# Kernel tuning notes

Hardware: AMD Instinct MI355X
Metric: run time of the kernel (lower is better)

## Reference

```python
import jax, jax.numpy as jnp
import numpy as np

N, F, HID, OUT, H = 4096, 128, 64, 16, 4
ALPHA = 0.2          # leaky relu slope
NEG = -9e15          # mask fill value (pyGAT convention)


def setup_inputs() -> dict:
    key = jax.random.key(0)
    ks = jax.random.split(key, 8)
    x = jax.random.normal(ks[0], (N, F), dtype=jnp.float32)
    adj = jax.random.randint(ks[1], (N, N), 0, 2, dtype=jnp.int32)
    s = lambda *sh: 0.1
    W_in = jax.random.normal(ks[2], (H, F, F), dtype=jnp.float32) * 0.1
    a_in = jax.random.normal(ks[3], (H, 2 * F), dtype=jnp.float32) * 0.1
    W_hid = jax.random.normal(ks[4], (H, F * H, HID), dtype=jnp.float32) * 0.1
    a_hid = jax.random.normal(ks[5], (H, 2 * HID), dtype=jnp.float32) * 0.1
    W_out = jax.random.normal(ks[6], (HID * H, OUT), dtype=jnp.float32) * 0.1
    a_out = jax.random.normal(ks[7], (2 * OUT,), dtype=jnp.float32) * 0.1
    return {"x": x, "adj": adj, "W_in": W_in, "a_in": a_in,
            "W_hid": W_hid, "a_hid": a_hid, "W_out": W_out, "a_out": a_out}


def _multi_head_att(x, W, a, mask):
    """Dense multi-head GAT aggregation. x:[N,Fin], W:[H,Fin,D], a:[H,2D] -> [H,N,D]."""
    D = W.shape[-1]
    h = jnp.einsum('nf,hfd->hnd', x, W)                      # [H,N,D]
    f1 = jnp.einsum('hnd,hd->hn', h, a[:, :D])               # source scores
    f2 = jnp.einsum('hnd,hd->hn', h, a[:, D:])               # target scores
    e = jax.nn.leaky_relu(f1[:, :, None] + f2[:, None, :], ALPHA)  # [H,N,N]
    e = jnp.where(mask[None, :, :], e, NEG)
    att = jax.nn.softmax(e, axis=-1)
    return jnp.einsum('hnm,hmd->hnd', att, h)                # [H,N,D]


def _concat_heads(h):
    # [H,N,D] -> [N,H*D]
    Hh, n, d = h.shape
    return jnp.transpose(h, (1, 0, 2)).reshape(n, Hh * d)


def reference(x, adj, W_in, a_in, W_hid, a_hid, W_out, a_out):
    mask = adj > 0
    # input attention block: concat=True (ELU per head), identity skip (in==out dim)
    h1 = _multi_head_att(x, W_in, a_in, mask)                # [H,N,F]
    h1 = jax.nn.elu(h1 + x[None, :, :])                      # identity residual
    h1 = _concat_heads(h1)                                   # [N,H*F]
    # hidden attention block: concat=True
    h2 = _multi_head_att(h1, W_hid, a_hid, mask)             # [H,N,HID]
    h2 = _concat_heads(jax.nn.elu(h2))                       # [N,H*HID]
    # output attention layer: single head, concat=False (no ELU inside)
    h3 = _multi_head_att(h2, W_out[None], a_out[None], mask)[0]  # [N,OUT]
    return jax.nn.log_softmax(jax.nn.elu(h3), axis=1)
```

## Files before the change

kernel.cpp:

```cpp
#include <hip/hip_runtime.h>
#include <math.h>

#define NN 4096
#define FF 128
#define HH 4
#define HIDD 64
#define OUTD 16
#define MASKW (NN / 32)
#define ALPHA 0.2f

typedef __attribute__((ext_vector_type(8))) short short8;
typedef __attribute__((ext_vector_type(4))) float f32x4;

__device__ __forceinline__ ushort f2bf(float f) {
    unsigned u = __float_as_uint(f);
    return (ushort)((u + 0x7fffu + ((u >> 16) & 1u)) >> 16);
}
__device__ __forceinline__ float bf2f(ushort u) {
    return __uint_as_float((unsigned)u << 16);
}

__global__ void pack_mask_kernel(const int* __restrict__ adj, unsigned int* __restrict__ mb) {
    int t = blockIdx.x * 256 + threadIdx.x;
    int v = adj[t] > 0;
    unsigned long long bal = __ballot(v);
    if ((threadIdx.x & 63) == 0) {
        int w = t >> 5;
        mb[w] = (unsigned int)(bal & 0xffffffffULL);
        mb[w + 1] = (unsigned int)(bal >> 32);
    }
}

__global__ void cvt_kernel(const float* __restrict__ x, ushort* __restrict__ xb) {
    int e = (blockIdx.x * 256 + threadIdx.x) * 4;
    f32x4 v = *(const f32x4*)&x[e];
    unsigned lo = (unsigned)f2bf(v[0]) | ((unsigned)f2bf(v[1]) << 16);
    unsigned hi = (unsigned)f2bf(v[2]) | ((unsigned)f2bf(v[3]) << 16);
    uint2 p; p.x = lo; p.y = hi;
    *(uint2*)&xb[e] = p;
}

__global__ void wtprep_kernel(const float* __restrict__ W_in, const float* __restrict__ W_hid,
                              const float* __restrict__ W_out,
                              ushort* __restrict__ wt1, ushort* __restrict__ wt2,
                              ushort* __restrict__ wt3) {
    int idx = blockIdx.x * 256 + threadIdx.x;
    if (idx < 65536) {
        int k = idx & 127, n = (idx >> 7) & 127, hd = idx >> 14;
        wt1[idx] = f2bf(W_in[((size_t)hd * 128 + k) * 128 + n]);
    } else if (idx < 65536 + 131072) {
        int j = idx - 65536;
        int k = j & 511, n = (j >> 9) & 63, hd = j >> 15;
        wt2[j] = f2bf(W_hid[((size_t)hd * 512 + k) * 64 + n]);
    } else if (idx < 65536 + 131072 + 4096) {
        int j = idx - 196608;
        int k = j & 255, n = j >> 8;
        wt3[j] = f2bf(W_out[(size_t)k * 16 + n]);
    }
}

__global__ void vprep_kernel(const float* __restrict__ W_in, const float* __restrict__ a_in,
                             const float* __restrict__ W_hid, const float* __restrict__ a_hid,
                             const float* __restrict__ W_out, const float* __restrict__ a_out,
                             float* __restrict__ vbuf) {
    int idx = blockIdx.x * 256 + threadIdx.x;
    const float* Wr; const float* ar; int D; float* dst;
    if (idx < 1024) {
        int f = idx & 127, hd = (idx >> 7) & 3, s = idx >> 9;
        Wr = W_in + ((size_t)hd * 128 + f) * 128;
        ar = a_in + hd * 256 + s * 128;
        D = 128; dst = &vbuf[idx];
    } else if (idx < 1024 + 4096) {
        int j = idx - 1024;
        int f = j & 511, hd = (j >> 9) & 3, s = j >> 11;
        Wr = W_hid + ((size_t)hd * 512 + f) * 64;
        ar = a_hid + hd * 128 + s * 64;
        D = 64; dst = &vbuf[1024 + j];
    } else if (idx < 1024 + 4096 + 512) {
        int j = idx - 5120;
        int f = j & 255, s = j >> 8;
        Wr = W_out + (size_t)f * 16;
        ar = a_out + s * 16;
        D = 16; dst = &vbuf[5120 + j];
    } else return;
    float s = 0.f;
    for (int d = 0; d < D; d++) s += Wr[d] * ar[d];
    *dst = s;
}

template <typename T, int K, int H>
__global__ __launch_bounds__(256) void score_kernel(const T* __restrict__ A,
                                                    const float* __restrict__ v,
                                                    float* __restrict__ f1,
                                                    float* __restrict__ f2) {
    int wv = blockIdx.x * 4 + (threadIdx.x >> 6);
    int lane = threadIdx.x & 63;
    int hd = wv >> 12;
    int i = wv & (NN - 1);
    const T* ar = A + (size_t)i * K;
    const float* v1r = v + (size_t)hd * K;
    const float* v2r = v + (size_t)(H + hd) * K;
    float s1 = 0.f, s2 = 0.f;
    for (int f = lane; f < K; f += 64) {
        float av;
        if constexpr (sizeof(T) == 2) av = bf2f(((const ushort*)ar)[f]);
        else av = ((const float*)ar)[f];
        s1 += av * v1r[f];
        s2 += av * v2r[f];
    }
#pragma unroll
    for (int o = 32; o > 0; o >>= 1) {
        s1 += __shfl_down(s1, o);
        s2 += __shfl_down(s2, o);
    }
    if (lane == 0) { f1[wv] = s1; f2[wv] = s2; }
}

__global__ void gmax_kernel(const float* __restrict__ f2, float* __restrict__ gmax) {
    int hd = blockIdx.x;
    const float* p = f2 + (size_t)hd * NN;
    float m = -1e30f;
    for (int i = threadIdx.x; i < NN; i += 256) m = fmaxf(m, p[i]);
    __shared__ float sm[4];
#pragma unroll
    for (int off = 32; off > 0; off >>= 1) m = fmaxf(m, __shfl_down(m, off));
    if ((threadIdx.x & 63) == 0) sm[threadIdx.x >> 6] = m;
    __syncthreads();
    if (threadIdx.x == 0) gmax[hd] = fmaxf(fmaxf(sm[0], sm[1]), fmaxf(sm[2], sm[3]));
}

template <int K, int N, int CFG>
__global__ __launch_bounds__(256) void proj_mfma_kernel(const ushort* __restrict__ A,
                                                        const ushort* __restrict__ WT,
                                                        ushort* __restrict__ hT) {
    constexpr int NT = (CFG == 0) ? (N / 64) : (N / 16);
    __shared__ ushort ts[4][NT * 16][20];
    const int hd = blockIdx.y;
    const int t = threadIdx.x;
    const int w = t >> 6, lane = t & 63, ln = lane & 15, g = lane >> 4, g8 = g * 8;
    const int i0 = (CFG == 0) ? blockIdx.x * 16 : blockIdx.x * 64 + w * 16;
    const int n0 = (CFG == 0) ? w * (N / 4) : 0;
    const ushort* WTh = WT + (size_t)hd * N * K;
    ushort* hTh = hT + (size_t)hd * N * NN;
    f32x4 acc[NT];
#pragma unroll
    for (int n = 0; n < NT; n++) acc[n] = (f32x4)(0.f);
    const ushort* arow = A + (size_t)(i0 + ln) * K + g8;
#pragma unroll
    for (int k0 = 0; k0 < K; k0 += 32) {
        short8 aF = *(const short8*)&arow[k0];
#pragma unroll
        for (int n = 0; n < NT; n++) {
            short8 bF = *(const short8*)&WTh[(size_t)(n0 + n * 16 + ln) * K + k0 + g8];
            acc[n] = __builtin_amdgcn_mfma_f32_16x16x32_bf16(aF, bF, acc[n], 0, 0, 0);
        }
    }
#pragma unroll
    for (int n = 0; n < NT; n++) {
        unsigned lo = (unsigned)f2bf(acc[n][0]) | ((unsigned)f2bf(acc[n][1]) << 16);
        unsigned hi = (unsigned)f2bf(acc[n][2]) | ((unsigned)f2bf(acc[n][3]) << 16);
        uint2 p; p.x = lo; p.y = hi;
        *(uint2*)&ts[w][n * 16 + ln][g * 4] = p;
    }
#pragma unroll
    for (int n = 0; n < NT; n++) {
        int d = lane >> 2, ip = lane & 3;
        uint2 rv = *(uint2*)&ts[w][n * 16 + d][ip * 4];
        *(uint2*)&hTh[(size_t)(n0 + n * 16 + d) * NN + i0 + ip * 4] = rv;
    }
}

template <int D>
__global__ __launch_bounds__(256) void agg3_kernel(const ushort* __restrict__ hT,
                                                   const float* __restrict__ f1,
                                                   const float* __restrict__ f2,
                                                   const float* __restrict__ gmax,
                                                   const unsigned int* __restrict__ mb,
                                                   float* __restrict__ pacc,
                                                   float* __restrict__ plsum) {
    constexpr int NT = D / 16;
    constexpr int NC = D / 64;
    __shared__ ushort hs[D][40];
    const int hd = blockIdx.z;
    const int js = blockIdx.y;
    const int jlen = NN / gridDim.y;
    const int jb = js * jlen, je = jb + jlen;
    const int t = threadIdx.x;
    const int w = t >> 6;
    const int lane = t & 63;
    const int ln = lane & 15;
    const int g = lane >> 4;
    const int g8 = g * 8;
    const int i0 = blockIdx.x * 64 + w * 16;
    const ushort* hTh = hT + (size_t)hd * D * NN;

    const float f1v = f1[hd * NN + i0 + ln];
    const float gm = gmax[hd];
    float mi = f1v + gm;
    mi = fmaxf(mi, ALPHA * mi);
    const float L2E = 1.442695040888963f;
    const float cexp = -mi * L2E;

    f32x4 acc[NT];
#pragma unroll
    for (int n = 0; n < NT; n++) acc[n] = (f32x4)(0.f);
    float lsum = 0.f;
    const float* f2h = f2 + hd * NN;
    const unsigned* mrow = mb + (size_t)(i0 + ln) * MASKW;

    int srow[NC], scol[NC];
#pragma unroll
    for (int c = 0; c < NC; c++) {
        int ch = t + c * 256;
        srow[c] = ch >> 2;
        scol[c] = (ch & 3) * 8;
    }
    uint4 st[NC];
#pragma unroll
    for (int c = 0; c < NC; c++)
        st[c] = *(const uint4*)&hTh[(size_t)srow[c] * NN + jb + scol[c]];
    unsigned mw = mrow[jb >> 5];
    f32x4 fA = *(const f32x4*)&f2h[jb + g8];
    f32x4 fB = *(const f32x4*)&f2h[jb + g8 + 4];

    for (int j0 = jb; j0 < je; j0 += 32) {
        __syncthreads();
#pragma unroll
        for (int c = 0; c < NC; c++) *(uint4*)&hs[srow[c]][scol[c]] = st[c];
        __syncthreads();
        const bool more = (j0 + 32) < je;
        if (more) {
#pragma unroll
            for (int c = 0; c < NC; c++)
                st[c] = *(const uint4*)&hTh[(size_t)srow[c] * NN + j0 + 32 + scol[c]];
        }
        unsigned bits = (mw >> g8) & 0xffu;
        f32x4 cA = fA, cB = fB;
        if (more) {
            mw = mrow[(j0 + 32) >> 5];
            fA = *(const f32x4*)&f2h[j0 + 32 + g8];
            fB = *(const f32x4*)&f2h[j0 + 32 + g8 + 4];
        }
        unsigned au[4];
#pragma unroll
        for (int tp = 0; tp < 4; tp++) {
            unsigned pu[2];
#pragma unroll
            for (int q = 0; q < 2; q++) {
                int tt = tp * 2 + q;
                float f2t = (tt < 4) ? cA[tt] : cB[tt - 4];
                float e = f1v + f2t;
                e = fmaxf(e, ALPHA * e);
                float p = ((bits >> tt) & 1u) ? __builtin_amdgcn_exp2f(e * L2E + cexp) : 0.f;
                pu[q] = __float_as_uint(p) & 0xffff0000u;
                lsum += __uint_as_float(pu[q]);
            }
            au[tp] = (pu[0] >> 16) | pu[1];
        }
        union { unsigned u[4]; short8 s; } aF;
#pragma unroll
        for (int q = 0; q < 4; q++) aF.u[q] = au[q];
#pragma unroll
        for (int n = 0; n < NT; n++) {
            short8 bF = *(const short8*)&hs[n * 16 + ln][g8];
            acc[n] = __builtin_amdgcn_mfma_f32_16x16x32_bf16(aF.s, bF, acc[n], 0, 0, 0);
        }
    }
    lsum += __shfl_xor(lsum, 16);
    lsum += __shfl_xor(lsum, 32);
    const size_t pbase = ((size_t)js * HH + hd) * NN;
    if (g == 0) plsum[pbase + i0 + ln] = lsum;
    float* pb = pacc + pbase * D;
#pragma unroll
    for (int n = 0; n < NT; n++) {
#pragma unroll
        for (int r = 0; r < 4; r++) {
            pb[(size_t)(i0 + g * 4 + r) * D + n * 16 + ln] = acc[n][r];
        }
    }
}

template <int D, int EPI>
__global__ __launch_bounds__(256) void combine_kernel(const float* __restrict__ pacc,
                                                      const float* __restrict__ plsum,
                                                      const float* __restrict__ xres,
                                                      ushort* __restrict__ out,
                                                      int ncols, int JS) {
    const int hd = blockIdx.y;
    const int e = (blockIdx.x * 256 + threadIdx.x) * 4;
    const int row = e / D;
    const int col = e % D;
    f32x4 s = (f32x4)(0.f);
    float l = 0.f;
    for (int js = 0; js < JS; js++) {
        const size_t pbase = ((size_t)js * HH + hd) * NN;
        s += *(const f32x4*)&pacc[(pbase + row) * D + col];
        l += plsum[pbase + row];
    }
    const float inv = 1.f / l;
    f32x4 xv;
    if (EPI == 1) xv = *(const f32x4*)&xres[(size_t)row * D + col];
    float o[4];
#pragma unroll
    for (int k = 0; k < 4; k++) {
        float v = s[k] * inv;
        if (EPI == 1) v += xv[k];
        if (EPI >= 1) v = v > 0.f ? v : (__expf(v) - 1.f);
        o[k] = v;
    }
    unsigned lo = (unsigned)f2bf(o[0]) | ((unsigned)f2bf(o[1]) << 16);
    unsigned hi = (unsigned)f2bf(o[2]) | ((unsigned)f2bf(o[3]) << 16);
    uint2 p; p.x = lo; p.y = hi;
    *(uint2*)&out[(size_t)row * ncols + hd * D + col] = p;
}

template <int D, int EPI>
__global__ __launch_bounds__(256) void agg2_kernel(const ushort* __restrict__ hT,
                                                   const float* __restrict__ f1,
                                                   const float* __restrict__ f2,
                                                   const float* __restrict__ gmax,
                                                   const unsigned int* __restrict__ mb,
                                                   const float* __restrict__ xres,
                                                   ushort* __restrict__ out, int ncols) {
    constexpr int NT = D / 16;
    constexpr int NC = D / 64;
    __shared__ ushort hs[D][40];
    const int hd = blockIdx.z;
    const int t = threadIdx.x;
    const int w = t >> 6;
    const int lane = t & 63;
    const int ln = lane & 15;
    const int g = lane >> 4;
    const int g8 = g * 8;
    const int i0 = blockIdx.x * 64 + w * 16;
    const ushort* hTh = hT + (size_t)hd * D * NN;
    const float f1v = f1[hd * NN + i0 + ln];
    const float gm = gmax[hd];
    float mi = f1v + gm;
    mi = fmaxf(mi, ALPHA * mi);
    const float L2E = 1.442695040888963f;
    const float cexp = -mi * L2E;
    f32x4 acc[NT];
#pragma unroll
    for (int n = 0; n < NT; n++) acc[n] = (f32x4)(0.f);
    float lsum = 0.f;
    const float* f2h = f2 + hd * NN;
    const unsigned* mrow = mb + (size_t)(i0 + ln) * MASKW;
    int srow[NC], scol[NC];
#pragma unroll
    for (int c = 0; c < NC; c++) {
        int ch = t + c * 256;
        srow[c] = ch >> 2;
        scol[c] = (ch & 3) * 8;
    }
    uint4 st[NC];
#pragma unroll
    for (int c = 0; c < NC; c++)
        st[c] = *(const uint4*)&hTh[(size_t)srow[c] * NN + scol[c]];
    unsigned mw = mrow[0];
    f32x4 fA = *(const f32x4*)&f2h[g8];
    f32x4 fB = *(const f32x4*)&f2h[g8 + 4];
    for (int j0 = 0; j0 < NN; j0 += 32) {
        __syncthreads();
#pragma unroll
        for (int c = 0; c < NC; c++) *(uint4*)&hs[srow[c]][scol[c]] = st[c];
        __syncthreads();
        const bool more = (j0 + 32) < NN;
        if (more) {
#pragma unroll
            for (int c = 0; c < NC; c++)
                st[c] = *(const uint4*)&hTh[(size_t)srow[c] * NN + j0 + 32 + scol[c]];
        }
        unsigned bits = (mw >> g8) & 0xffu;
        f32x4 cA = fA, cB = fB;
        if (more) {
            mw = mrow[(j0 + 32) >> 5];
            fA = *(const f32x4*)&f2h[j0 + 32 + g8];
            fB = *(const f32x4*)&f2h[j0 + 32 + g8 + 4];
        }
        unsigned au[4];
#pragma unroll
        for (int tp = 0; tp < 4; tp++) {
            unsigned pu[2];
#pragma unroll
            for (int q = 0; q < 2; q++) {
                int tt = tp * 2 + q;
                float f2t = (tt < 4) ? cA[tt] : cB[tt - 4];
                float e = f1v + f2t;
                e = fmaxf(e, ALPHA * e);
                float p = ((bits >> tt) & 1u) ? __builtin_amdgcn_exp2f(e * L2E + cexp) : 0.f;
                pu[q] = __float_as_uint(p) & 0xffff0000u;
                lsum += __uint_as_float(pu[q]);
            }
            au[tp] = (pu[0] >> 16) | pu[1];
        }
        union { unsigned u[4]; short8 s; } aF;
#pragma unroll
        for (int q = 0; q < 4; q++) aF.u[q] = au[q];
#pragma unroll
        for (int n = 0; n < NT; n++) {
            short8 bF = *(const short8*)&hs[n * 16 + ln][g8];
            acc[n] = __builtin_amdgcn_mfma_f32_16x16x32_bf16(aF.s, bF, acc[n], 0, 0, 0);
        }
    }
    lsum += __shfl_xor(lsum, 16);
    lsum += __shfl_xor(lsum, 32);
    const float linv = 1.f / lsum;
#pragma unroll
    for (int n = 0; n < NT; n++) {
#pragma unroll
        for (int r = 0; r < 4; r++) {
            float invr = __shfl(linv, (g << 2) + r);
            float v = acc[n][r] * invr;
            int row = i0 + g * 4 + r;
            int col = n * 16 + ln;
            if (EPI == 1) v += xres[(size_t)row * D + col];
            if (EPI >= 1) v = v > 0.f ? v : (__expf(v) - 1.f);
            out[(size_t)row * ncols + hd * D + col] = f2bf(v);
        }
    }
}

template <int D, int EPI, int NW>
__global__ __launch_bounds__(NW * 64) void agg_mfma_kernel(const ushort* __restrict__ hT,
                                                           const float* __restrict__ f1,
                                                           const float* __restrict__ f2,
                                                           const float* __restrict__ gmax,
                                                           const unsigned int* __restrict__ mb,
                                                           const float* __restrict__ xres,
                                                           float* __restrict__ out, int ncols) {
    constexpr int NT = D / 16;
    static_assert(NW == 1 || NT == 1, "j-split only for single-tile D");
    const int hd = blockIdx.z;
    const int i0 = blockIdx.x * 16;
    const int w = threadIdx.x >> 6;
    const int lane = threadIdx.x & 63;
    const int ln = lane & 15;
    const int g = lane >> 4;
    const int g8 = g * 8;
    const ushort* hTh = hT + (size_t)hd * D * NN;
    const float f1v = f1[hd * NN + i0 + ln];
    const float gm = gmax[hd];
    float mi = f1v + gm;
    mi = fmaxf(mi, ALPHA * mi);
    f32x4 acc[NT];
#pragma unroll
    for (int n = 0; n < NT; n++) acc[n] = (f32x4)(0.f);
    float lsum = 0.f;
    const float* f2h = f2 + hd * NN;
    const unsigned* mrow = mb + (size_t)(i0 + ln) * MASKW;
    const int jbeg = w * (NN / NW), jend = jbeg + NN / NW;

    for (int j0 = jbeg; j0 < jend; j0 += 32) {
        unsigned bits = (mrow[j0 >> 5] >> g8) & 0xffu;
        f32x4 fA = *(const f32x4*)&f2h[j0 + g8];
        f32x4 fB = *(const f32x4*)&f2h[j0 + g8 + 4];
        short8 aF;
#pragma unroll
        for (int t = 0; t < 8; t++) {
            float f2t = (t < 4) ? fA[t] : fB[t - 4];
            float e = f1v + f2t;
            e = fmaxf(e, ALPHA * e);
            float p = ((bits >> t) & 1u) ? __expf(e - mi) : 0.f;
            ushort pb = f2bf(p);
            aF[t] = (short)pb;
            lsum += __uint_as_float((unsigned)pb << 16);
        }
#pragma unroll
        for (int n = 0; n < NT; n++) {
            short8 bF = *(const short8*)&hTh[(size_t)(n * 16 + ln) * NN + j0 + g8];
            acc[n] = __builtin_amdgcn_mfma_f32_16x16x32_bf16(aF, bF, acc[n], 0, 0, 0);
        }
    }
    lsum += __shfl_xor(lsum, 16);
    lsum += __shfl_xor(lsum, 32);

    float accF[NT][4];
    float ltot;
    __shared__ float accL[NW][16][17];
    __shared__ float lsL[NW][16];
    if constexpr (NW == 1) {
#pragma unroll
        for (int n = 0; n < NT; n++)
#pragma unroll
            for (int r = 0; r < 4; r++) accF[n][r] = acc[n][r];
        ltot = lsum;
    } else {
#pragma unroll
        for (int r = 0; r < 4; r++) accL[w][g * 4 + r][ln] = acc[0][r];
        if (lane < 16) lsL[w][lane] = lsum;
        __syncthreads();
        if (w != 0) return;
#pragma unroll
        for (int r = 0; r < 4; r++) {
            float s = 0.f;
            for (int ww = 0; ww < NW; ww++) s += accL[ww][g * 4 + r][ln];
            accF[0][r] = s;
        }
        float s = 0.f;
        for (int ww = 0; ww < NW; ww++) s += lsL[ww][ln];
        ltot = s;
    }
    const float linv = 1.f / ltot;
#pragma unroll
    for (int n = 0; n < NT; n++) {
#pragma unroll
        for (int r = 0; r < 4; r++) {
            float invr = __shfl(linv, (g << 2) + r);
            float v = accF[n][r] * invr;
            int row = i0 + g * 4 + r;
            int col = n * 16 + ln;
            if (EPI == 1) v += xres[(size_t)row * D + col];
            if (EPI >= 1) v = v > 0.f ? v : (__expf(v) - 1.f);
            out[(size_t)row * ncols + hd * D + col] = v;
        }
    }
}

__global__ void final_kernel(const float* __restrict__ h3, float* __restrict__ out) {
    int i = blockIdx.x * 256 + threadIdx.x;
    if (i >= NN) return;
    float v[OUTD];
    float mx = -1e30f;
#pragma unroll
    for (int k = 0; k < OUTD; k++) {
        float e = h3[(size_t)i * OUTD + k];
        e = e > 0.f ? e : (__expf(e) - 1.f);
        v[k] = e;
        mx = fmaxf(mx, e);
    }
    float s = 0.f;
#pragma unroll
    for (int k = 0; k < OUTD; k++) s += __expf(v[k] - mx);
    float ls = logf(s);
#pragma unroll
    for (int k = 0; k < OUTD; k++) out[(size_t)i * OUTD + k] = v[k] - mx - ls;
}

extern "C" void kernel_launch(void* const* d_in, const int* in_sizes, int n_in,
                              void* d_out, int out_size, void* d_ws, size_t ws_size,
                              hipStream_t stream) {
    const float* x = (const float*)d_in[0];
    const int* adj = (const int*)d_in[1];
    const float* W_in = (const float*)d_in[2];
    const float* a_in = (const float*)d_in[3];
    const float* W_hid = (const float*)d_in[4];
    const float* a_hid = (const float*)d_in[5];
    const float* W_out = (const float*)d_in[6];
    const float* a_out = (const float*)d_in[7];
    float* out = (float*)d_out;

    char* w = (char*)d_ws;
    unsigned int* mb = (unsigned int*)w;  w += (size_t)NN * MASKW * 4;
    ushort* hT = (ushort*)w;              w += (size_t)HH * NN * FF * 2;
    ushort* xb16 = (ushort*)w;            w += (size_t)NN * FF * 2;
    ushort* cat1b = (ushort*)w;           w += (size_t)NN * (HH * FF) * 2;
    ushort* cat2b = (ushort*)w;           w += (size_t)NN * (HH * HIDD) * 2;
    ushort* wt1 = (ushort*)w;             w += 65536 * 2;
    ushort* wt2 = (ushort*)w;             w += 131072 * 2;
    ushort* wt3 = (ushort*)w;             w += 4096 * 2;
    float* vbuf = (float*)w;              w += 5632 * 4;
    float* f1 = (float*)w;                w += (size_t)HH * NN * 4;
    float* f2 = (float*)w;                w += (size_t)HH * NN * 4;
    float* gm = (float*)w;                w += 256;
    float* h3 = (float*)w;                w += (size_t)NN * OUTD * 4;
    size_t base_used = (size_t)(w - (char*)d_ws);

    int JS = 0;
    float* pacc = (float*)w;
    float* plsum = nullptr;
    {
        size_t per_js = (size_t)HH * NN * FF * 4;
        size_t ls_per_js = (size_t)HH * NN * 4;
        for (int cand = 4; cand >= 1; cand >>= 1) {
            size_t need = base_used + (size_t)cand * per_js + (size_t)(2 * cand) * ls_per_js + 1024;
            if (ws_size >= need) { JS = cand; break; }
        }
        if (JS) plsum = (float*)((char*)pacc + (size_t)JS * per_js);
    }
    const int JS2 = 2 * JS;

    hipLaunchKernelGGL(pack_mask_kernel, dim3(NN * NN / 256), dim3(256), 0, stream, adj, mb);
    hipLaunchKernelGGL(cvt_kernel, dim3(NN * FF / 1024), dim3(256), 0, stream, x, xb16);
    hipLaunchKernelGGL(wtprep_kernel, dim3(784), dim3(256), 0, stream,
                       W_in, W_hid, W_out, wt1, wt2, wt3);
    hipLaunchKernelGGL(vprep_kernel, dim3(22), dim3(256), 0, stream,
                       W_in, a_in, W_hid, a_hid, W_out, a_out, vbuf);

    hipLaunchKernelGGL((proj_mfma_kernel<FF, FF, 0>), dim3(NN / 16, HH), dim3(256), 0, stream,
                       xb16, wt1, hT);
    hipLaunchKernelGGL((score_kernel<float, FF, HH>), dim3(HH * NN / 4), dim3(256), 0, stream,
                       x, vbuf, f1, f2);
    hipLaunchKernelGGL(gmax_kernel, dim3(HH), dim3(256), 0, stream, f2, gm);
    if (JS) {
        hipLaunchKernelGGL((agg3_kernel<FF>), dim3(NN / 64, JS, HH), dim3(256), 0, stream,
                           hT, f1, f2, gm, mb, pacc, plsum);
        hipLaunchKernelGGL((combine_kernel<FF, 1>), dim3(NN * FF / 1024, HH), dim3(256), 0, stream,
                           pacc, plsum, x, cat1b, HH * FF, JS);
    } else {
        hipLaunchKernelGGL((agg2_kernel<FF, 1>), dim3(NN / 64, 1, HH), dim3(256), 0, stream,
                           hT, f1, f2, gm, mb, x, cat1b, HH * FF);
    }

    hipLaunchKernelGGL((proj_mfma_kernel<HH * FF, HIDD, 0>), dim3(NN / 16, HH), dim3(256), 0, stream,
                       cat1b, wt2, hT);
    hipLaunchKernelGGL((score_kernel<ushort, HH * FF, HH>), dim3(HH * NN / 4), dim3(256), 0, stream,
                       cat1b, vbuf + 1024, f1, f2);
    hipLaunchKernelGGL(gmax_kernel, dim3(HH), dim3(256), 0, stream, f2, gm);
    if (JS) {
        hipLaunchKernelGGL((agg3_kernel<HIDD>), dim3(NN / 64, JS2, HH), dim3(256), 0, stream,
                           hT, f1, f2, gm, mb, pacc, plsum);
        hipLaunchKernelGGL((combine_kernel<HIDD, 2>), dim3(NN * HIDD / 1024, HH), dim3(256), 0, stream,
                           pacc, plsum, (const float*)nullptr, cat2b, HH * HIDD, JS2);
    } else {
        hipLaunchKernelGGL((agg2_kernel<HIDD, 2>), dim3(NN / 64, 1, HH), dim3(256), 0, stream,
                           hT, f1, f2, gm, mb, (const float*)nullptr, cat2b, HH * HIDD);
    }

    hipLaunchKernelGGL((proj_mfma_kernel<HH * HIDD, OUTD, 1>), dim3(NN / 64, 1), dim3(256), 0, stream,
                       cat2b, wt3, hT);
    hipLaunchKernelGGL((score_kernel<ushort, HH * HIDD, 1>), dim3(NN / 4), dim3(256), 0, stream,
                       cat2b, vbuf + 5120, f1, f2);
    hipLaunchKernelGGL(gmax_kernel, dim3(1), dim3(256), 0, stream, f2, gm);
    hipLaunchKernelGGL((agg_mfma_kernel<OUTD, 0, 4>), dim3(NN / 16, 1, 1), dim3(256), 0, stream,
                       hT, f1, f2, gm, mb, (const float*)nullptr, h3, OUTD);

    hipLaunchKernelGGL(final_kernel, dim3(NN / 256), dim3(256), 0, stream, h3, out);
}
```

Before: 339.3 us.

## Restructure split-K aggregation with XCD-aware block mapping and fragment-ordered LDS

The aggregation kernel becomes agg4: a 1D grid whose block index is remapped so each XCD handles contiguous (split, head) combos, which should improve L2 locality of hT and mask reads. LDS is laid out directly in MFMA fragment order, avoiding padded row indexing. Each iteration now processes 64 columns (two MFMA k-steps per barrier pair), halving synchronisations. The split count can go up to 8, and partial accumulators are stored in a tiled 16x16 layout that combine reads back. Costs include more register pressure, f2 and mask loads that are no longer prefetched, and more workspace for partial sums.

```diff
diff --git a/kernel.cpp b/kernel.cpp
--- a/kernel.cpp
+++ b/kernel.cpp
@@ -171,27 +171,43 @@
 }
 
 template <int D>
-__global__ __launch_bounds__(256) void agg3_kernel(const ushort* __restrict__ hT,
+__global__ __launch_bounds__(256) void agg4_kernel(const ushort* __restrict__ hT,
                                                    const float* __restrict__ f1,
                                                    const float* __restrict__ f2,
                                                    const float* __restrict__ gmax,
                                                    const unsigned int* __restrict__ mb,
                                                    float* __restrict__ pacc,
-                                                   float* __restrict__ plsum) {
+                                                   float* __restrict__ plsum,
+                                                   int lgJS) {
     constexpr int NT = D / 16;
-    constexpr int NC = D / 64;
-    __shared__ ushort hs[D][40];
-    const int hd = blockIdx.z;
-    const int js = blockIdx.y;
-    const int jlen = NN / gridDim.y;
+    constexpr int CHS = NT * 64;
+    constexpr int NC = NT / 2;
+    __shared__ ushort hs[2 * CHS * 8];
+    const int JS = 1 << lgJS;
+    const int jlen = NN >> lgJS;
+    const int combos = JS * HH;
+    const int bid = blockIdx.x;
+    int ibk, combo;
+    if (combos >= 8) {
+        int xcd = bid & 7;
+        int sid = bid >> 3;
+        combo = xcd * (combos >> 3) + (sid >> 6);
+        ibk = sid & 63;
+    } else {
+        ibk = bid & 63;
+        combo = bid >> 6;
+    }
+    const int js = combo & (JS - 1);
+    const int hd = combo >> lgJS;
     const int jb = js * jlen, je = jb + jlen;
+
     const int t = threadIdx.x;
     const int w = t >> 6;
     const int lane = t & 63;
     const int ln = lane & 15;
     const int g = lane >> 4;
     const int g8 = g * 8;
-    const int i0 = blockIdx.x * 64 + w * 16;
+    const int i0 = ibk * 64 + w * 16;
     const ushort* hTh = hT + (size_t)hd * D * NN;
 
     const float f1v = f1[hd * NN + i0 + ln];
@@ -208,74 +224,75 @@
     const float* f2h = f2 + hd * NN;
     const unsigned* mrow = mb + (size_t)(i0 + ln) * MASKW;
 
-    int srow[NC], scol[NC];
+    int srow[NC], scol[NC], soff[NC];
 #pragma unroll
     for (int c = 0; c < NC; c++) {
         int ch = t + c * 256;
-        srow[c] = ch >> 2;
-        scol[c] = (ch & 3) * 8;
+        int s = ch / CHS;
+        int inner = ch - s * CHS;
+        int n = inner >> 6;
+        int l = inner & 63;
+        srow[c] = n * 16 + (l & 15);
+        scol[c] = s * 32 + (l >> 4) * 8;
+        soff[c] = ch * 8;
     }
     uint4 st[NC];
 #pragma unroll
     for (int c = 0; c < NC; c++)
         st[c] = *(const uint4*)&hTh[(size_t)srow[c] * NN + jb + scol[c]];
-    unsigned mw = mrow[jb >> 5];
-    f32x4 fA = *(const f32x4*)&f2h[jb + g8];
-    f32x4 fB = *(const f32x4*)&f2h[jb + g8 + 4];
-
-    for (int j0 = jb; j0 < je; j0 += 32) {
+
+    for (int j0 = jb; j0 < je; j0 += 64) {
         __syncthreads();
 #pragma unroll
-        for (int c = 0; c < NC; c++) *(uint4*)&hs[srow[c]][scol[c]] = st[c];
+        for (int c = 0; c < NC; c++) *(uint4*)&hs[soff[c]] = st[c];
         __syncthreads();
-        const bool more = (j0 + 32) < je;
+        const bool more = (j0 + 64) < je;
         if (more) {
 #pragma unroll
             for (int c = 0; c < NC; c++)
-                st[c] = *(const uint4*)&hTh[(size_t)srow[c] * NN + j0 + 32 + scol[c]];
-        }
-        unsigned bits = (mw >> g8) & 0xffu;
-        f32x4 cA = fA, cB = fB;
-        if (more) {
-            mw = mrow[(j0 + 32) >> 5];
-            fA = *(const f32x4*)&f2h[j0 + 32 + g8];
-            fB = *(const f32x4*)&f2h[j0 + 32 + g8 + 4];
-        }
-        unsigned au[4];
-#pragma unroll
-        for (int tp = 0; tp < 4; tp++) {
-            unsigned pu[2];
-#pragma unroll
-            for (int q = 0; q < 2; q++) {
-                int tt = tp * 2 + q;
-                float f2t = (tt < 4) ? cA[tt] : cB[tt - 4];
-                float e = f1v + f2t;
-                e = fmaxf(e, ALPHA * e);
-                float p = ((bits >> tt) & 1u) ? __builtin_amdgcn_exp2f(e * L2E + cexp) : 0.f;
-                pu[q] = __float_as_uint(p) & 0xffff0000u;
-                lsum += __uint_as_float(pu[q]);
+                st[c] = *(const uint4*)&hTh[(size_t)srow[c] * NN + j0 + 64 + scol[c]];
+        }
+        uint2 mw2 = *(const uint2*)&mrow[j0 >> 5];
+#pragma unroll
+        for (int s = 0; s < 2; s++) {
+            unsigned bits = ((s ? mw2.y : mw2.x) >> g8) & 0xffu;
+            f32x4 cA = *(const f32x4*)&f2h[j0 + s * 32 + g8];
+            f32x4 cB = *(const f32x4*)&f2h[j0 + s * 32 + g8 + 4];
+            unsigned au[4];
+#pragma unroll
+            for (int tp = 0; tp < 4; tp++) {
+                unsigned pu[2];
+#pragma unroll
+                for (int q = 0; q < 2; q++) {
+                    int tt = tp * 2 + q;
+                    float f2t = (tt < 4) ? cA[tt] : cB[tt - 4];
+                    float e = f1v + f2t;
+                    e = fmaxf(e, ALPHA * e);
+                    float p = ((bits >> tt) & 1u) ? __builtin_amdgcn_exp2f(e * L2E + cexp) : 0.f;
+                    pu[q] = __float_as_uint(p) & 0xffff0000u;
+                    lsum += __uint_as_float(pu[q]);
+                }
+                au[tp] = (pu[0] >> 16) | pu[1];
             }
-            au[tp] = (pu[0] >> 16) | pu[1];
-        }
-        union { unsigned u[4]; short8 s; } aF;
-#pragma unroll
-        for (int q = 0; q < 4; q++) aF.u[q] = au[q];
-#pragma unroll
-        for (int n = 0; n < NT; n++) {
-            short8 bF = *(const short8*)&hs[n * 16 + ln][g8];
-            acc[n] = __builtin_amdgcn_mfma_f32_16x16x32_bf16(aF.s, bF, acc[n], 0, 0, 0);
+            union { unsigned u[4]; short8 v; } aF;
+#pragma unroll
+            for (int q = 0; q < 4; q++) aF.u[q] = au[q];
+#pragma unroll
+            for (int n = 0; n < NT; n++) {
+                short8 bF = *(const short8*)&hs[((s * NT + n) * 64 + lane) * 8];
+                acc[n] = __builtin_amdgcn_mfma_f32_16x16x32_bf16(aF.v, bF, acc[n], 0, 0, 0);
+            }
         }
     }
     lsum += __shfl_xor(lsum, 16);
     lsum += __shfl_xor(lsum, 32);
-    const size_t pbase = ((size_t)js * HH + hd) * NN;
-    if (g == 0) plsum[pbase + i0 + ln] = lsum;
-    float* pb = pacc + pbase * D;
+    if (g == 0) plsum[(size_t)combo * NN + i0 + ln] = lsum;
+    float* pb = pacc + ((size_t)combo * NN + i0) * D;
 #pragma unroll
     for (int n = 0; n < NT; n++) {
 #pragma unroll
         for (int r = 0; r < 4; r++) {
-            pb[(size_t)(i0 + g * 4 + r) * D + n * 16 + ln] = acc[n][r];
+            pb[n * 256 + (g * 4 + r) * 16 + ln] = acc[n][r];
         }
     }
 }
@@ -290,12 +307,13 @@
     const int e = (blockIdx.x * 256 + threadIdx.x) * 4;
     const int row = e / D;
     const int col = e % D;
+    const size_t fidx = ((size_t)(row & ~15)) * D + (col >> 4) * 256 + (row & 15) * 16 + (col & 15);
     f32x4 s = (f32x4)(0.f);
     float l = 0.f;
     for (int js = 0; js < JS; js++) {
-        const size_t pbase = ((size_t)js * HH + hd) * NN;
-        s += *(const f32x4*)&pacc[(pbase + row) * D + col];
-        l += plsum[pbase + row];
+        const size_t cix = (size_t)(hd * JS + js) * NN;
+        s += *(const f32x4*)&pacc[cix * D + fidx];
+        l += plsum[cix + row];
     }
     const float inv = 1.f / l;
     f32x4 xv;
@@ -566,19 +584,22 @@
     float* h3 = (float*)w;                w += (size_t)NN * OUTD * 4;
     size_t base_used = (size_t)(w - (char*)d_ws);
 
-    int JS = 0;
+    int lgJS = -1;
     float* pacc = (float*)w;
     float* plsum = nullptr;
     {
         size_t per_js = (size_t)HH * NN * FF * 4;
         size_t ls_per_js = (size_t)HH * NN * 4;
-        for (int cand = 4; cand >= 1; cand >>= 1) {
-            size_t need = base_used + (size_t)cand * per_js + (size_t)(2 * cand) * ls_per_js + 1024;
-            if (ws_size >= need) { JS = cand; break; }
-        }
-        if (JS) plsum = (float*)((char*)pacc + (size_t)JS * per_js);
-    }
-    const int JS2 = 2 * JS;
+        for (int lg = 3; lg >= 0; lg--) {
+            size_t cand = (size_t)1 << lg;
+            size_t need = base_used + cand * per_js + 8 * ls_per_js + 1024;
+            if (ws_size >= need) { lgJS = lg; break; }
+        }
+        if (lgJS >= 0) plsum = (float*)((char*)pacc + ((size_t)1 << lgJS) * per_js);
+    }
+    const int JS = (lgJS >= 0) ? (1 << lgJS) : 0;
+    const int lgJS2 = (lgJS >= 3) ? 3 : lgJS + 1;
+    const int JS2 = 1 << lgJS2;
 
     hipLaunchKernelGGL(pack_mask_kernel, dim3(NN * NN / 256), dim3(256), 0, stream, adj, mb);
     hipLaunchKernelGGL(cvt_kernel, dim3(NN * FF / 1024), dim3(256), 0, stream, x, xb16);
@@ -593,8 +614,8 @@
                        x, vbuf, f1, f2);
     hipLaunchKernelGGL(gmax_kernel, dim3(HH), dim3(256), 0, stream, f2, gm);
     if (JS) {
-        hipLaunchKernelGGL((agg3_kernel<FF>), dim3(NN / 64, JS, HH), dim3(256), 0, stream,
-                           hT, f1, f2, gm, mb, pacc, plsum);
+        hipLaunchKernelGGL((agg4_kernel<FF>), dim3(64 * JS * HH), dim3(256), 0, stream,
+                           hT, f1, f2, gm, mb, pacc, plsum, lgJS);
         hipLaunchKernelGGL((combine_kernel<FF, 1>), dim3(NN * FF / 1024, HH), dim3(256), 0, stream,
                            pacc, plsum, x, cat1b, HH * FF, JS);
     } else {
@@ -608,8 +629,8 @@
                        cat1b, vbuf + 1024, f1, f2);
     hipLaunchKernelGGL(gmax_kernel, dim3(HH), dim3(256), 0, stream, f2, gm);
     if (JS) {
-        hipLaunchKernelGGL((agg3_kernel<HIDD>), dim3(NN / 64, JS2, HH), dim3(256), 0, stream,
-                           hT, f1, f2, gm, mb, pacc, plsum);
+        hipLaunchKernelGGL((agg4_kernel<HIDD>), dim3(64 * JS2 * HH), dim3(256), 0, stream,
+                           hT, f1, f2, gm, mb, pacc, plsum, lgJS2);
         hipLaunchKernelGGL((combine_kernel<HIDD, 2>), dim3(NN * HIDD / 1024, HH), dim3(256), 0, stream,
                            pacc, plsum, (const float*)nullptr, cat2b, HH * HIDD, JS2);
     } else {
```

Measured after the change: 409.8 us. +20.8%, slower.

## Replace split-K aggregation and combine with in-block wave split-K agg5 kernel

Applied to the files above, without the earlier changes.

Replaces the agg3 and combine path with a single agg5 kernel. Each block handles 32 rows of one head, and its four waves each take a quarter of the neighbor range, reducing through shared memory. The kernel drops the LDS staging of hT and loads B fragments directly from global memory. It computes the softmax denominator with an extra MFMA against a ones vector, so the row sum uses the same bf16-rounded values as the numerator. Block ids are remapped so each XCD works on one head, which removes the partial-accumulator global round trip and one launch per layer, at the cost of uncoalesced direct global loads and lower per-block parallelism.

```diff
diff --git a/kernel.cpp b/kernel.cpp
--- a/kernel.cpp
+++ b/kernel.cpp
@@ -170,152 +170,8 @@
     }
 }
 
-template <int D>
-__global__ __launch_bounds__(256) void agg3_kernel(const ushort* __restrict__ hT,
-                                                   const float* __restrict__ f1,
-                                                   const float* __restrict__ f2,
-                                                   const float* __restrict__ gmax,
-                                                   const unsigned int* __restrict__ mb,
-                                                   float* __restrict__ pacc,
-                                                   float* __restrict__ plsum) {
-    constexpr int NT = D / 16;
-    constexpr int NC = D / 64;
-    __shared__ ushort hs[D][40];
-    const int hd = blockIdx.z;
-    const int js = blockIdx.y;
-    const int jlen = NN / gridDim.y;
-    const int jb = js * jlen, je = jb + jlen;
-    const int t = threadIdx.x;
-    const int w = t >> 6;
-    const int lane = t & 63;
-    const int ln = lane & 15;
-    const int g = lane >> 4;
-    const int g8 = g * 8;
-    const int i0 = blockIdx.x * 64 + w * 16;
-    const ushort* hTh = hT + (size_t)hd * D * NN;
-
-    const float f1v = f1[hd * NN + i0 + ln];
-    const float gm = gmax[hd];
-    float mi = f1v + gm;
-    mi = fmaxf(mi, ALPHA * mi);
-    const float L2E = 1.442695040888963f;
-    const float cexp = -mi * L2E;
-
-    f32x4 acc[NT];
-#pragma unroll
-    for (int n = 0; n < NT; n++) acc[n] = (f32x4)(0.f);
-    float lsum = 0.f;
-    const float* f2h = f2 + hd * NN;
-    const unsigned* mrow = mb + (size_t)(i0 + ln) * MASKW;
-
-    int srow[NC], scol[NC];
-#pragma unroll
-    for (int c = 0; c < NC; c++) {
-        int ch = t + c * 256;
-        srow[c] = ch >> 2;
-        scol[c] = (ch & 3) * 8;
-    }
-    uint4 st[NC];
-#pragma unroll
-    for (int c = 0; c < NC; c++)
-        st[c] = *(const uint4*)&hTh[(size_t)srow[c] * NN + jb + scol[c]];
-    unsigned mw = mrow[jb >> 5];
-    f32x4 fA = *(const f32x4*)&f2h[jb + g8];
-    f32x4 fB = *(const f32x4*)&f2h[jb + g8 + 4];
-
-    for (int j0 = jb; j0 < je; j0 += 32) {
-        __syncthreads();
-#pragma unroll
-        for (int c = 0; c < NC; c++) *(uint4*)&hs[srow[c]][scol[c]] = st[c];
-        __syncthreads();
-        const bool more = (j0 + 32) < je;
-        if (more) {
-#pragma unroll
-            for (int c = 0; c < NC; c++)
-                st[c] = *(const uint4*)&hTh[(size_t)srow[c] * NN + j0 + 32 + scol[c]];
-        }
-        unsigned bits = (mw >> g8) & 0xffu;
-        f32x4 cA = fA, cB = fB;
-        if (more) {
-            mw = mrow[(j0 + 32) >> 5];
-            fA = *(const f32x4*)&f2h[j0 + 32 + g8];
-            fB = *(const f32x4*)&f2h[j0 + 32 + g8 + 4];
-        }
-        unsigned au[4];
-#pragma unroll
-        for (int tp = 0; tp < 4; tp++) {
-            unsigned pu[2];
-#pragma unroll
-            for (int q = 0; q < 2; q++) {
-                int tt = tp * 2 + q;
-                float f2t = (tt < 4) ? cA[tt] : cB[tt - 4];
-                float e = f1v + f2t;
-                e = fmaxf(e, ALPHA * e);
-                float p = ((bits >> tt) & 1u) ? __builtin_amdgcn_exp2f(e * L2E + cexp) : 0.f;
-                pu[q] = __float_as_uint(p) & 0xffff0000u;
-                lsum += __uint_as_float(pu[q]);
-            }
-            au[tp] = (pu[0] >> 16) | pu[1];
-        }
-        union { unsigned u[4]; short8 s; } aF;
-#pragma unroll
-        for (int q = 0; q < 4; q++) aF.u[q] = au[q];
-#pragma unroll
-        for (int n = 0; n < NT; n++) {
-            short8 bF = *(const short8*)&hs[n * 16 + ln][g8];
-            acc[n] = __builtin_amdgcn_mfma_f32_16x16x32_bf16(aF.s, bF, acc[n], 0, 0, 0);
-        }
-    }
-    lsum += __shfl_xor(lsum, 16);
-    lsum += __shfl_xor(lsum, 32);
-    const size_t pbase = ((size_t)js * HH + hd) * NN;
-    if (g == 0) plsum[pbase + i0 + ln] = lsum;
-    float* pb = pacc + pbase * D;
-#pragma unroll
-    for (int n = 0; n < NT; n++) {
-#pragma unroll
-        for (int r = 0; r < 4; r++) {
-            pb[(size_t)(i0 + g * 4 + r) * D + n * 16 + ln] = acc[n][r];
-        }
-    }
-}
-
 template <int D, int EPI>
-__global__ __launch_bounds__(256) void combine_kernel(const float* __restrict__ pacc,
-                                                      const float* __restrict__ plsum,
-                                                      const float* __restrict__ xres,
-                                                      ushort* __restrict__ out,
-                                                      int ncols, int JS) {
-    const int hd = blockIdx.y;
-    const int e = (blockIdx.x * 256 + threadIdx.x) * 4;
-    const int row = e / D;
-    const int col = e % D;
-    f32x4 s = (f32x4)(0.f);
-    float l = 0.f;
-    for (int js = 0; js < JS; js++) {
-        const size_t pbase = ((size_t)js * HH + hd) * NN;
-        s += *(const f32x4*)&pacc[(pbase + row) * D + col];
-        l += plsum[pbase + row];
-    }
-    const float inv = 1.f / l;
-    f32x4 xv;
-    if (EPI == 1) xv = *(const f32x4*)&xres[(size_t)row * D + col];
-    float o[4];
-#pragma unroll
-    for (int k = 0; k < 4; k++) {
-        float v = s[k] * inv;
-        if (EPI == 1) v += xv[k];
-        if (EPI >= 1) v = v > 0.f ? v : (__expf(v) - 1.f);
-        o[k] = v;
-    }
-    unsigned lo = (unsigned)f2bf(o[0]) | ((unsigned)f2bf(o[1]) << 16);
-    unsigned hi = (unsigned)f2bf(o[2]) | ((unsigned)f2bf(o[3]) << 16);
-    uint2 p; p.x = lo; p.y = hi;
-    *(uint2*)&out[(size_t)row * ncols + hd * D + col] = p;
-}
-
-template <int D, int EPI>
-__global__ __launch_bounds__(256) void agg2_kernel(const ushort* __restrict__ hT,
+__global__ __launch_bounds__(256) void agg5_kernel(const ushort* __restrict__ hT,
                                                    const float* __restrict__ f1,
                                                    const float* __restrict__ f2,
                                                    const float* __restrict__ gmax,
@@ -323,100 +179,138 @@
                                                    const float* __restrict__ xres,
                                                    ushort* __restrict__ out, int ncols) {
     constexpr int NT = D / 16;
-    constexpr int NC = D / 64;
-    __shared__ ushort hs[D][40];
-    const int hd = blockIdx.z;
+    __shared__ float red[3][2 * NT * 272];
+    __shared__ float redl[3][2][16];
+    const int bid = blockIdx.x;
+    const int xcd = bid & 7;
+    const int hd = xcd >> 1;
+    const int ig = ((xcd & 1) << 6) + (bid >> 3);
+    const int i0 = ig * 32;
     const int t = threadIdx.x;
     const int w = t >> 6;
     const int lane = t & 63;
     const int ln = lane & 15;
     const int g = lane >> 4;
     const int g8 = g * 8;
-    const int i0 = blockIdx.x * 64 + w * 16;
     const ushort* hTh = hT + (size_t)hd * D * NN;
-    const float f1v = f1[hd * NN + i0 + ln];
+    const float* f2h = f2 + hd * NN;
     const float gm = gmax[hd];
-    float mi = f1v + gm;
-    mi = fmaxf(mi, ALPHA * mi);
     const float L2E = 1.442695040888963f;
-    const float cexp = -mi * L2E;
-    f32x4 acc[NT];
-#pragma unroll
-    for (int n = 0; n < NT; n++) acc[n] = (f32x4)(0.f);
-    float lsum = 0.f;
-    const float* f2h = f2 + hd * NN;
-    const unsigned* mrow = mb + (size_t)(i0 + ln) * MASKW;
-    int srow[NC], scol[NC];
-#pragma unroll
-    for (int c = 0; c < NC; c++) {
-        int ch = t + c * 256;
-        srow[c] = ch >> 2;
-        scol[c] = (ch & 3) * 8;
-    }
-    uint4 st[NC];
-#pragma unroll
-    for (int c = 0; c < NC; c++)
-        st[c] = *(const uint4*)&hTh[(size_t)srow[c] * NN + scol[c]];
-    unsigned mw = mrow[0];
-    f32x4 fA = *(const f32x4*)&f2h[g8];
-    f32x4 fB = *(const f32x4*)&f2h[g8 + 4];
-    for (int j0 = 0; j0 < NN; j0 += 32) {
-        __syncthreads();
-#pragma unroll
-        for (int c = 0; c < NC; c++) *(uint4*)&hs[srow[c]][scol[c]] = st[c];
-        __syncthreads();
-        const bool more = (j0 + 32) < NN;
-        if (more) {
-#pragma unroll
-            for (int c = 0; c < NC; c++)
-                st[c] = *(const uint4*)&hTh[(size_t)srow[c] * NN + j0 + 32 + scol[c]];
-        }
-        unsigned bits = (mw >> g8) & 0xffu;
-        f32x4 cA = fA, cB = fB;
-        if (more) {
-            mw = mrow[(j0 + 32) >> 5];
-            fA = *(const f32x4*)&f2h[j0 + 32 + g8];
-            fB = *(const f32x4*)&f2h[j0 + 32 + g8 + 4];
-        }
-        unsigned au[4];
+    float f1v[2], cexp[2];
+#pragma unroll
+    for (int it = 0; it < 2; it++) {
+        float f = f1[hd * NN + i0 + it * 16 + ln];
+        f1v[it] = f;
+        float mi = f + gm;
+        mi = fmaxf(mi, ALPHA * mi);
+        cexp[it] = -mi * L2E;
+    }
+    f32x4 acc[2][NT];
+#pragma unroll
+    for (int it = 0; it < 2; it++)
+#pragma unroll
+        for (int n = 0; n < NT; n++) acc[it][n] = (f32x4)(0.f);
+    f32x4 accl[2];
+    accl[0] = (f32x4)(0.f);
+    accl[1] = (f32x4)(0.f);
+    short8 bONE;
+#pragma unroll
+    for (int q = 0; q < 8; q++) bONE[q] = (short)0x3F80;
+
+    const unsigned* mrow0 = mb + (size_t)(i0 + ln) * MASKW;
+    const unsigned* mrow1 = mrow0 + 16 * MASKW;
+    const int jb = w * (NN / 4), je = jb + NN / 4;
+    unsigned m0 = mrow0[jb >> 5], m1 = mrow1[jb >> 5];
+    f32x4 cA = *(const f32x4*)&f2h[jb + g8];
+    f32x4 cB = *(const f32x4*)&f2h[jb + g8 + 4];
+
+    for (int j0 = jb; j0 < je; j0 += 32) {
+        short8 bf[NT];
+#pragma unroll
+        for (int n = 0; n < NT; n++)
+            bf[n] = *(const short8*)&hTh[(size_t)(n * 16 + ln) * NN + j0 + g8];
+        unsigned cm0 = m0, cm1 = m1;
+        f32x4 fA = cA, fB = cB;
+        if (j0 + 32 < je) {
+            m0 = mrow0[(j0 + 32) >> 5];
+            m1 = mrow1[(j0 + 32) >> 5];
+            cA = *(const f32x4*)&f2h[j0 + 32 + g8];
+            cB = *(const f32x4*)&f2h[j0 + 32 + g8 + 4];
+        }
+        unsigned bits0 = (cm0 >> g8) & 0xffu;
+        unsigned bits1 = (cm1 >> g8) & 0xffu;
+        union { unsigned u[4]; short8 v; } aF[2];
 #pragma unroll
         for (int tp = 0; tp < 4; tp++) {
-            unsigned pu[2];
+            unsigned pu[2][2];
 #pragma unroll
             for (int q = 0; q < 2; q++) {
                 int tt = tp * 2 + q;
-                float f2t = (tt < 4) ? cA[tt] : cB[tt - 4];
-                float e = f1v + f2t;
-                e = fmaxf(e, ALPHA * e);
-                float p = ((bits >> tt) & 1u) ? __builtin_amdgcn_exp2f(e * L2E + cexp) : 0.f;
-                pu[q] = __float_as_uint(p) & 0xffff0000u;
-                lsum += __uint_as_float(pu[q]);
+                float f2t = (tt < 4) ? fA[tt] : fB[tt - 4];
+#pragma unroll
+                for (int it = 0; it < 2; it++) {
+                    float e = f1v[it] + f2t;
+                    e = fmaxf(e, ALPHA * e);
+                    unsigned b = it ? bits1 : bits0;
+                    float p = ((b >> tt) & 1u) ? __builtin_amdgcn_exp2f(e * L2E + cexp[it]) : 0.f;
+                    pu[it][q] = __float_as_uint(p) & 0xffff0000u;
+                }
             }
-            au[tp] = (pu[0] >> 16) | pu[1];
-        }
-        union { unsigned u[4]; short8 s; } aF;
-#pragma unroll
-        for (int q = 0; q < 4; q++) aF.u[q] = au[q];
+            aF[0].u[tp] = (pu[0][0] >> 16) | pu[0][1];
+            aF[1].u[tp] = (pu[1][0] >> 16) | pu[1][1];
+        }
+#pragma unroll
+        for (int it = 0; it < 2; it++) {
+#pragma unroll
+            for (int n = 0; n < NT; n++)
+                acc[it][n] = __builtin_amdgcn_mfma_f32_16x16x32_bf16(aF[it].v, bf[n], acc[it][n], 0, 0, 0);
+            accl[it] = __builtin_amdgcn_mfma_f32_16x16x32_bf16(aF[it].v, bONE, accl[it], 0, 0, 0);
+        }
+    }
+    if (w != 0) {
+        float* rb = red[w - 1];
+#pragma unroll
+        for (int it = 0; it < 2; it++) {
+#pragma unroll
+            for (int n = 0; n < NT; n++)
+#pragma unroll
+                for (int r = 0; r < 4; r++)
+                    rb[(it * NT + n) * 272 + (g * 4 + r) * 17 + ln] = acc[it][n][r];
+            if (ln == 0) {
+#pragma unroll
+                for (int r = 0; r < 4; r++) redl[w - 1][it][g * 4 + r] = accl[it][r];
+            }
+        }
+    }
+    __syncthreads();
+    if (w != 0) return;
+#pragma unroll
+    for (int it = 0; it < 2; it++) {
+        f32x4 lt = accl[it];
+#pragma unroll
+        for (int b = 0; b < 3; b++)
+#pragma unroll
+            for (int r = 0; r < 4; r++) lt[r] += redl[b][it][g * 4 + r];
+        f32x4 linv;
+#pragma unroll
+        for (int r = 0; r < 4; r++) linv[r] = 1.f / lt[r];
 #pragma unroll
         for (int n = 0; n < NT; n++) {
-            short8 bF = *(const short8*)&hs[n * 16 + ln][g8];
-            acc[n] = __builtin_amdgcn_mfma_f32_16x16x32_bf16(aF.s, bF, acc[n], 0, 0, 0);
-        }
-    }
-    lsum += __shfl_xor(lsum, 16);
-    lsum += __shfl_xor(lsum, 32);
-    const float linv = 1.f / lsum;
-#pragma unroll
-    for (int n = 0; n < NT; n++) {
-#pragma unroll
-        for (int r = 0; r < 4; r++) {
-            float invr = __shfl(linv, (g << 2) + r);
-            float v = acc[n][r] * invr;
-            int row = i0 + g * 4 + r;
-            int col = n * 16 + ln;
-            if (EPI == 1) v += xres[(size_t)row * D + col];
-            if (EPI >= 1) v = v > 0.f ? v : (__expf(v) - 1.f);
-            out[(size_t)row * ncols + hd * D + col] = f2bf(v);
+            f32x4 s = acc[it][n];
+#pragma unroll
+            for (int b = 0; b < 3; b++)
+#pragma unroll
+                for (int r = 0; r < 4; r++)
+                    s[r] += red[b][(it * NT + n) * 272 + (g * 4 + r) * 17 + ln];
+#pragma unroll
+            for (int r = 0; r < 4; r++) {
+                float v = s[r] * linv[r];
+                int row = i0 + it * 16 + g * 4 + r;
+                int col = n * 16 + ln;
+                if (EPI == 1) v += xres[(size_t)row * D + col];
+                if (EPI >= 1) v = v > 0.f ? v : (__expf(v) - 1.f);
+                out[(size_t)row * ncols + hd * D + col] = f2bf(v);
+            }
         }
     }
 }
@@ -564,21 +458,6 @@
     float* f2 = (float*)w;                w += (size_t)HH * NN * 4;
     float* gm = (float*)w;                w += 256;
     float* h3 = (float*)w;                w += (size_t)NN * OUTD * 4;
-    size_t base_used = (size_t)(w - (char*)d_ws);
-
-    int JS = 0;
-    float* pacc = (float*)w;
-    float* plsum = nullptr;
-    {
-        size_t per_js = (size_t)HH * NN * FF * 4;
-        size_t ls_per_js = (size_t)HH * NN * 4;
-        for (int cand = 4; cand >= 1; cand >>= 1) {
-            size_t need = base_used + (size_t)cand * per_js + (size_t)(2 * cand) * ls_per_js + 1024;
-            if (ws_size >= need) { JS = cand; break; }
-        }
-        if (JS) plsum = (float*)((char*)pacc + (size_t)JS * per_js);
-    }
-    const int JS2 = 2 * JS;
 
     hipLaunchKernelGGL(pack_mask_kernel, dim3(NN * NN / 256), dim3(256), 0, stream, adj, mb);
     hipLaunchKernelGGL(cvt_kernel, dim3(NN * FF / 1024), dim3(256), 0, stream, x, xb16);
@@ -592,30 +471,16 @@
     hipLaunchKernelGGL((score_kernel<float, FF, HH>), dim3(HH * NN / 4), dim3(256), 0, stream,
                        x, vbuf, f1, f2);
     hipLaunchKernelGGL(gmax_kernel, dim3(HH), dim3(256), 0, stream, f2, gm);
-    if (JS) {
-        hipLaunchKernelGGL((agg3_kernel<FF>), dim3(NN / 64, JS, HH), dim3(256), 0, stream,
-                           hT, f1, f2, gm, mb, pacc, plsum);
-        hipLaunchKernelGGL((combine_kernel<FF, 1>), dim3(NN * FF / 1024, HH), dim3(256), 0, stream,
-                           pacc, plsum, x, cat1b, HH * FF, JS);
-    } else {
-        hipLaunchKernelGGL((agg2_kernel<FF, 1>), dim3(NN / 64, 1, HH), dim3(256), 0, stream,
-                           hT, f1, f2, gm, mb, x, cat1b, HH * FF);
-    }
+    hipLaunchKernelGGL((agg5_kernel<FF, 1>), dim3((NN / 32) * HH), dim3(256), 0, stream,
+                       hT, f1, f2, gm, mb, x, cat1b, HH * FF);
 
     hipLaunchKernelGGL((proj_mfma_kernel<HH * FF, HIDD, 0>), dim3(NN / 16, HH), dim3(256), 0, stream,
                        cat1b, wt2, hT);
     hipLaunchKernelGGL((score_kernel<ushort, HH * FF, HH>), dim3(HH * NN / 4), dim3(256), 0, stream,
                        cat1b, vbuf + 1024, f1, f2);
     hipLaunchKernelGGL(gmax_kernel, dim3(HH), dim3(256), 0, stream, f2, gm);
-    if (JS) {
-        hipLaunchKernelGGL((agg3_kernel<HIDD>), dim3(NN / 64, JS2, HH), dim3(256), 0, stream,
-                           hT, f1, f2, gm, mb, pacc, plsum);
-        hipLaunchKernelGGL((combine_kernel<HIDD, 2>), dim3(NN * HIDD / 1024, HH), dim3(256), 0, stream,
-                           pacc, plsum, (const float*)nullptr, cat2b, HH * HIDD, JS2);
-    } else {
-        hipLaunchKernelGGL((agg2_kernel<HIDD, 2>), dim3(NN / 64, 1, HH), dim3(256), 0, stream,
-                           hT, f1, f2, gm, mb, (const float*)nullptr, cat2b, HH * HIDD);
-    }
+    hipLaunchKernelGGL((agg5_kernel<HIDD, 2>), dim3((NN / 32) * HH), dim3(256), 0, stream,
+                       hT, f1, f2, gm, mb, (const float*)nullptr, cat2b, HH * HIDD);
 
     hipLaunchKernelGGL((proj_mfma_kernel<HH * HIDD, OUTD, 1>), dim3(NN / 64, 1), dim3(256), 0, stream,
                        cat2b, wt3, hT);
```

Result: slower. 358.1 us (+5.5%).
